# Kernel optimization log

Measured on AMD Instinct MI355X. Metric: run time of the kernel, lower is better.

The kernel has to match this reference:

```python
import jax, jax.numpy as jnp
import numpy as np

B, D, A = 512, 32, 18          # batch, n_latent_dims (= n_heads), n_actions
FED, AED = 128, 64             # factor/action embed dims
VD = FED + AED                 # vdim = 192
KD = VD                        # kdim (key_embed_dim=None -> vdim)
HID = 256                      # per-head MLP hidden size
H = D                          # n_heads = n_latent_dims


def setup_inputs() -> dict:
    key = jax.random.key(0)
    ks = jax.random.split(key, 20)
    s = lambda i, shape: jax.random.normal(ks[i], shape, dtype=jnp.float32) * 0.05
    return {
        "features": jax.random.normal(ks[0], (B, D), dtype=jnp.float32),
        "actions": jax.random.uniform(ks[1], (B, A), dtype=jnp.float32),
        # linear projections (stored as [in, out], i.e. torch weight.T)
        "Wq": s(2, (A, KD)),  "bq": s(3, (KD,)),      # action_query_projection
        "Wk": s(4, (D, KD)),  "bk": s(5, (KD,)),      # factor_key_projection
        "Wav": s(6, (A, AED)), "bav": s(7, (AED,)),   # action_val_projection
        "Wfv": s(8, (D, FED)), "bfv": s(9, (FED,)),   # factor_val_projection
        # per-head input MLPs: vdim -> HID -> vdim (ReLU)
        "W1": s(10, (H, VD, HID)), "b1": s(11, (H, HID)),
        "W2": s(12, (H, HID, VD)), "b2": s(13, (H, VD)),
        # per-head output MLPs: vdim -> HID -> 1 (ReLU)
        "W1o": s(14, (H, VD, HID)), "b1o": s(15, (H, HID)),
        "W2o": s(16, (H, HID)),     "b2o": s(17, (H,)),
    }


def reference(features, actions, Wq, bq, Wk, bk, Wav, bav, Wfv, bfv,
              W1, b1, W2, b2, W1o, b1o, W2o, b2o):
    z, a = features, actions
    # diag_embed(z) row i = z_i * e_i, so Linear(diag_embed(z))[..., i, :] = z_i * W.T[i] + b.
    # z is expanded identically across heads, so factor embeds/keys are head-independent.
    factor_embeds = z[:, :, None] * Wfv[None] + bfv          # [B, D, FED]
    keys = z[:, :, None] * Wk[None] + bk                     # [B, D, KD]
    queries = a @ Wq + bq                                    # [B, KD]
    action_embeds = a @ Wav + bav                            # [B, AED]

    # concat factor vals with broadcast action vals -> [B, D, VD]
    cv = jnp.concatenate(
        [factor_embeds, jnp.broadcast_to(action_embeds[:, None, :], (B, D, AED))], axis=-1)

    # per-head input MLPs (ReLU), batched over heads via einsum
    h = jax.nn.relu(jnp.einsum('bdv,hvk->bhdk', cv, W1) + b1[None, :, None, :])
    values = jnp.einsum('bhdk,hkv->bhdv', h, W2) + b2[None, :, None, :]  # [B,H,D,VD]

    # attention: single query vs D keys; head-independent weights
    scores = (keys @ queries[:, :, None])[..., 0] / jnp.sqrt(jnp.float32(KD))  # [B, D]
    w = jax.nn.softmax(scores, axis=-1)                       # [B, D]
    attn_out = jnp.einsum('bd,bhdv->bhv', w, values)          # [B, H, VD]

    # per-head output MLPs (ReLU) -> scalar effect per head
    h2 = jax.nn.relu(jnp.einsum('bhv,hvk->bhk', attn_out, W1o) + b1o[None])
    effect = jnp.einsum('bhk,hk->bh', h2, W2o) + b2o[None]    # [B, H]

    attn_weights = jnp.broadcast_to(w[:, None, :], (B, H, D))  # [B, H, D]
    return effect, attn_weights
```

## Files before the change

kernel.cpp:

```cpp
#include <hip/hip_runtime.h>
#include <hip/hip_bf16.h>


typedef __attribute__((ext_vector_type(8))) short bf16x8;
typedef __attribute__((ext_vector_type(4))) short bf16x4;
typedef __attribute__((ext_vector_type(4))) float f32x4;

__device__ __forceinline__ short f2bf(float x) {
  unsigned u = __float_as_uint(x);
  u += 0x7fffu + ((u >> 16) & 1u);
  return (short)(u >> 16);
}

__global__ __launch_bounds__(256) void kA_prep(
    const float* __restrict__ feat, const float* __restrict__ act,
    const float* __restrict__ Wq, const float* __restrict__ bq,
    const float* __restrict__ Wk,
    const float* __restrict__ Wav, const float* __restrict__ bav,
    const float* __restrict__ Wfv, const float* __restrict__ bfv,
    const float* __restrict__ W1, const float* __restrict__ b1,
    const float* __restrict__ W2, const float* __restrict__ b2,
    const float* __restrict__ W1o, const float* __restrict__ b1o,
    float* __restrict__ ws_w, float* __restrict__ ws_U,
    float* __restrict__ ws_c0, unsigned short* __restrict__ ws_Mbf,
    float* __restrict__ ws_c1, float* __restrict__ ws_W1g,
    float* __restrict__ out_aw) {
  __shared__ float sh[8448];
  const int bx = blockIdx.x;
  const int t = threadIdx.x;

  if (bx < 64) {
    const int b0 = bx * 8;
    float* sWk = sh;
    float* sA  = sh + 6144;
    float* sQk = sh + 6320;
    float* sW  = sh + 6944;
#pragma unroll
    for (int i = 0; i < 24; ++i) {
      const int idx = i * 256 + t;
      sWk[(idx % 192) * 32 + (idx / 192)] = Wk[idx];
    }
    if (t < 144) sA[t] = act[b0 * 18 + t];
    __syncthreads();
    for (int o = t; o < 608; o += 256) {
      const int j = o >> 5, d = o & 31;
      const float* arow = (j < 18) ? (Wq + j * 192) : bq;
      float acc = 0.f;
      for (int c = 0; c < 192; ++c) acc += arow[c] * sWk[c * 32 + d];
      sQk[o] = acc;
    }
    __syncthreads();
    {
      const int bi = t >> 5, d = t & 31;
      float dot = sQk[18 * 32 + d];
#pragma unroll
      for (int j = 0; j < 18; ++j) dot += sA[bi * 18 + j] * sQk[j * 32 + d];
      const float z = feat[b0 * 32 + t];
      float sc = z * dot * 0.07216878364870322f;
      float mx = sc;
#pragma unroll
      for (int off = 16; off >= 1; off >>= 1) mx = fmaxf(mx, __shfl_xor(mx, off, 64));
      const float e = __expf(sc - mx);
      float s = e;
#pragma unroll
      for (int off = 16; off >= 1; off >>= 1) s += __shfl_xor(s, off, 64);
      const float w = e / s;
      ws_w[b0 * 32 + t] = w;
      sW[t] = w;
    }
    __syncthreads();
#pragma unroll
    for (int i = 0; i < 32; ++i)
      out_aw[b0 * 1024 + i * 256 + t] = sW[(i >> 2) * 32 + (t & 31)];

  } else if (bx < 224) {
    const int r = bx - 64;
    const int h = r / 5, dt = r % 5;
    float* sF = sh;
    if (dt < 4) {
#pragma unroll
      for (int i = 0; i < 4; ++i) sF[i * 256 + t] = Wfv[dt * 1024 + i * 256 + t];
    } else {
      if (t < 128) sF[t] = bfv[t];
    }
    __syncthreads();
    if (dt < 4) {
      float acc[8];
#pragma unroll
      for (int dd = 0; dd < 8; ++dd) acc[dd] = 0.f;
#pragma unroll 4
      for (int fc = 0; fc < 32; ++fc) {
        float w1v[4];
#pragma unroll
        for (int u = 0; u < 4; ++u) w1v[u] = W1[(h * 192 + fc * 4 + u) * 256 + t];
#pragma unroll
        for (int dd = 0; dd < 8; ++dd) {
          float4 f4 = *(const float4*)(sF + dd * 128 + fc * 4);
          acc[dd] += f4.x * w1v[0] + f4.y * w1v[1] + f4.z * w1v[2] + f4.w * w1v[3];
        }
      }
#pragma unroll
      for (int dd = 0; dd < 8; ++dd)
        ws_U[(h * 32 + dt * 8 + dd) * 256 + t] = acc[dd];
    } else {
      float acc = b1[h * 256 + t];
      for (int fc = 0; fc < 32; ++fc) {
        float w1v[4];
#pragma unroll
        for (int u = 0; u < 4; ++u) w1v[u] = W1[(h * 192 + fc * 4 + u) * 256 + t];
        float4 f4 = *(const float4*)(sF + fc * 4);
        acc += f4.x * w1v[0] + f4.y * w1v[1] + f4.z * w1v[2] + f4.w * w1v[3];
      }
      for (int u = 0; u < 64; ++u)
        acc += bav[u] * W1[(h * 192 + 128 + u) * 256 + t];
      ws_c0[h * 256 + t] = acc;
    }

  } else if (bx < 736) {
    const int r = bx - 224;
    const int h = r >> 4, kt = r & 15;
    float* s = sh;
    if (t < 192) {
#pragma unroll
      for (int rr = 0; rr < 16; ++rr)
        s[rr * 200 + t] = W2[h * 49152 + kt * 3072 + rr * 192 + t];
    }
    __syncthreads();
    const int k2q = t >> 2, rq = t & 3;
    float acc[4][4];
#pragma unroll
    for (int r0 = 0; r0 < 4; ++r0)
#pragma unroll
      for (int c = 0; c < 4; ++c) acc[r0][c] = 0.f;
    float c1acc[4] = {0.f, 0.f, 0.f, 0.f};
    const float* W1op = W1o + h * 49152 + k2q * 4;
#pragma unroll 4
    for (int vc = 0; vc < 48; ++vc) {
      float w1q[4][4];
#pragma unroll
      for (int u = 0; u < 4; ++u) {
        float4 w4 = *(const float4*)(W1op + (vc * 4 + u) * 256);
        w1q[u][0] = w4.x; w1q[u][1] = w4.y; w1q[u][2] = w4.z; w1q[u][3] = w4.w;
      }
      float w2q[4][4];
#pragma unroll
      for (int r0 = 0; r0 < 4; ++r0) {
        float4 w2 = *(const float4*)(s + (rq * 4 + r0) * 200 + vc * 4);
        w2q[r0][0] = w2.x; w2q[r0][1] = w2.y; w2q[r0][2] = w2.z; w2q[r0][3] = w2.w;
      }
      float b2v[4];
#pragma unroll
      for (int u = 0; u < 4; ++u) b2v[u] = b2[h * 192 + vc * 4 + u];
#pragma unroll
      for (int u = 0; u < 4; ++u) {
#pragma unroll
        for (int c = 0; c < 4; ++c) c1acc[c] += b2v[u] * w1q[u][c];
#pragma unroll
        for (int r0 = 0; r0 < 4; ++r0)
#pragma unroll
          for (int c = 0; c < 4; ++c)
            acc[r0][c] += w2q[r0][u] * w1q[u][c];
      }
    }
#pragma unroll
    for (int c = 0; c < 4; ++c) {
      bf16x4 p;
#pragma unroll
      for (int r0 = 0; r0 < 4; ++r0) p[r0] = f2bf(acc[r0][c]);
      *(bf16x4*)(ws_Mbf + (size_t)(h * 256 + k2q * 4 + c) * 256 + kt * 16 + rq * 4) = p;
    }
    if (kt == 0 && rq == 0) {
#pragma unroll
      for (int c = 0; c < 4; ++c)
        ws_c1[h * 256 + k2q * 4 + c] = c1acc[c] + b1o[h * 256 + k2q * 4 + c];
    }

  } else {
    const int h = bx - 736;
    float accj[18];
#pragma unroll
    for (int j = 0; j < 18; ++j) accj[j] = 0.f;
#pragma unroll 4
    for (int u = 0; u < 64; ++u) {
      const float w1v = W1[(h * 192 + 128 + u) * 256 + t];
#pragma unroll
      for (int j = 0; j < 18; ++j)
        accj[j] += Wav[j * 64 + u] * w1v;
    }
#pragma unroll
    for (int j = 0; j < 18; ++j)
      ws_W1g[(h * 20 + j) * 256 + t] = accj[j];
    ws_W1g[(h * 20 + 18) * 256 + t] = 0.f;
    ws_W1g[(h * 20 + 19) * 256 + t] = 0.f;
  }
}

__global__ __launch_bounds__(256) void kB_main(
    const float* __restrict__ feat, const float* __restrict__ act,
    const float* __restrict__ ws_w, const float* __restrict__ ws_U,
    const float* __restrict__ ws_W1g, const float* __restrict__ ws_c0,
    const unsigned short* __restrict__ ws_Mbf, const float* __restrict__ ws_c1,
    const float* __restrict__ W2o, const float* __restrict__ b2o,
    float* __restrict__ out_eff) {
  const int bx = blockIdx.x;
  const int h = (bx & 7) * 4 + ((bx >> 3) & 3);
  const int bt = bx >> 5;
  const int b0 = bt * 16;
  const int t = threadIdx.x;

  __shared__ __align__(16) char smem[14208];
  short* sP   = (short*)smem;
  float* sA   = (float*)(smem + 8448);
  float* sZ   = (float*)(smem + 9728);
  float* sWw  = (float*)(smem + 11776);
  float* sRed = (float*)(smem + 13824);

  {
#pragma unroll
    for (int i = 0; i < 2; ++i) {
      sZ[i * 256 + t]  = feat[b0 * 32 + i * 256 + t];
      sWw[i * 256 + t] = ws_w[b0 * 32 + i * 256 + t];
    }
    for (int i = t; i < 320; i += 256) {
      const int row = i / 20, col = i - row * 20;
      sA[i] = (col < 18) ? act[(b0 + row) * 18 + col] : 0.f;
    }
  }
  __syncthreads();

  {
    const int bq = t >> 6, kg = t & 63;
    float g[4][4];

    {
      float4 c04 = *(const float4*)(ws_c0 + h * 256 + kg * 4);
#pragma unroll
      for (int r = 0; r < 4; ++r) {
        g[r][0] = c04.x; g[r][1] = c04.y; g[r][2] = c04.z; g[r][3] = c04.w;
      }
      const float* Wgp = ws_W1g + (h * 20) * 256 + kg * 4;
#pragma unroll
      for (int jc = 0; jc < 5; ++jc) {
        float w1q[4][4];
#pragma unroll
        for (int u = 0; u < 4; ++u) {
          float4 w4 = *(const float4*)(Wgp + (jc * 4 + u) * 256);
          w1q[u][0] = w4.x; w1q[u][1] = w4.y; w1q[u][2] = w4.z; w1q[u][3] = w4.w;
        }
        float a4[4][4];
#pragma unroll
        for (int r = 0; r < 4; ++r) {
          float4 av = *(const float4*)(sA + (bq * 4 + r) * 20 + jc * 4);
          a4[r][0] = av.x; a4[r][1] = av.y; a4[r][2] = av.z; a4[r][3] = av.w;
        }
#pragma unroll
        for (int u = 0; u < 4; ++u)
#pragma unroll
          for (int r = 0; r < 4; ++r)
#pragma unroll
            for (int c = 0; c < 4; ++c)
              g[r][c] += a4[r][u] * w1q[u][c];
      }
    }

    float acc[4][4];
#pragma unroll
    for (int r = 0; r < 4; ++r) {
      acc[r][0] = 0.f; acc[r][1] = 0.f; acc[r][2] = 0.f; acc[r][3] = 0.f;
    }
    const float* Up = ws_U + h * 8192 + kg * 4;
#pragma unroll
    for (int dc = 0; dc < 8; ++dc) {
      float uc[4][4];
#pragma unroll
      for (int dd = 0; dd < 4; ++dd) {
        float4 u4 = *(const float4*)(Up + (dc * 4 + dd) * 256);
        uc[dd][0] = u4.x; uc[dd][1] = u4.y; uc[dd][2] = u4.z; uc[dd][3] = u4.w;
      }
      float zr[4][4], wr[4][4];
#pragma unroll
      for (int r = 0; r < 4; ++r) {
        float4 z4 = *(const float4*)(sZ + (bq * 4 + r) * 32 + dc * 4);
        float4 w4 = *(const float4*)(sWw + (bq * 4 + r) * 32 + dc * 4);
        zr[r][0] = z4.x; zr[r][1] = z4.y; zr[r][2] = z4.z; zr[r][3] = z4.w;
        wr[r][0] = w4.x; wr[r][1] = w4.y; wr[r][2] = w4.z; wr[r][3] = w4.w;
      }
#pragma unroll
      for (int dd = 0; dd < 4; ++dd) {
#pragma unroll
        for (int r = 0; r < 4; ++r) {
#pragma unroll
          for (int c = 0; c < 4; ++c)
            acc[r][c] += wr[r][dd] * fmaxf(zr[r][dd] * uc[dd][c] + g[r][c], 0.f);
        }
      }
    }
#pragma unroll
    for (int r = 0; r < 4; ++r) {
      bf16x4 p;
#pragma unroll
      for (int c = 0; c < 4; ++c) p[c] = f2bf(acc[r][c]);
      *(bf16x4*)(sP + (bq * 4 + r) * 264 + kg * 4) = p;
    }
  }
  __syncthreads();

  {
    const int wv = t >> 6;
    const int lane = t & 63;
    const int quad = lane >> 4, l15 = lane & 15;

    f32x4 acc[4];
    const f32x4 zero = {0.f, 0.f, 0.f, 0.f};
#pragma unroll
    for (int nt = 0; nt < 4; ++nt) acc[nt] = zero;

    float c1r[4], w2r[4];
#pragma unroll
    for (int nt = 0; nt < 4; ++nt) {
      const int col = wv * 64 + nt * 16 + l15;
      c1r[nt] = ws_c1[h * 256 + col];
      w2r[nt] = W2o[h * 256 + col];
    }
    const unsigned short* Mp = ws_Mbf + (size_t)(h * 256 + wv * 64) * 256;

#pragma unroll
    for (int kc = 0; kc < 8; ++kc) {
      bf16x8 a0 = *(const bf16x8*)(sP + l15 * 264 + kc * 32 + quad * 8);
      bf16x8 bfr[4];
#pragma unroll
      for (int nt = 0; nt < 4; ++nt)
        bfr[nt] = *(const bf16x8*)(Mp + (nt * 16 + l15) * 256 + kc * 32 + quad * 8);
#pragma unroll
      for (int nt = 0; nt < 4; ++nt)
        acc[nt] = __builtin_amdgcn_mfma_f32_16x16x32_bf16(a0, bfr[nt], acc[nt], 0, 0, 0);
    }
#pragma unroll
    for (int r = 0; r < 4; ++r) {
      float s = fmaxf(acc[0][r] + c1r[0], 0.f) * w2r[0]
              + fmaxf(acc[1][r] + c1r[1], 0.f) * w2r[1]
              + fmaxf(acc[2][r] + c1r[2], 0.f) * w2r[2]
              + fmaxf(acc[3][r] + c1r[3], 0.f) * w2r[3];
      s += __shfl_xor(s, 1, 64);
      s += __shfl_xor(s, 2, 64);
      s += __shfl_xor(s, 4, 64);
      s += __shfl_xor(s, 8, 64);
      if (l15 == 0) sRed[(quad * 4 + r) * 4 + wv] = s;
    }
  }
  __syncthreads();
  if (t < 16) {
    float v = sRed[t * 4] + sRed[t * 4 + 1] + sRed[t * 4 + 2] + sRed[t * 4 + 3] + b2o[h];
    out_eff[(b0 + t) * 32 + h] = v;
  }
}

extern "C" void kernel_launch(void* const* d_in, const int* in_sizes, int n_in,
                              void* d_out, int out_size, void* d_ws, size_t ws_size,
                              hipStream_t stream) {
  const float* feat = (const float*)d_in[0];
  const float* act  = (const float*)d_in[1];
  const float* Wq   = (const float*)d_in[2];
  const float* bq   = (const float*)d_in[3];
  const float* Wk   = (const float*)d_in[4];
  const float* Wav  = (const float*)d_in[6];
  const float* bav  = (const float*)d_in[7];
  const float* Wfv  = (const float*)d_in[8];
  const float* bfv  = (const float*)d_in[9];
  const float* W1   = (const float*)d_in[10];
  const float* b1   = (const float*)d_in[11];
  const float* W2   = (const float*)d_in[12];
  const float* b2   = (const float*)d_in[13];
  const float* W1o  = (const float*)d_in[14];
  const float* b1o  = (const float*)d_in[15];
  const float* W2o  = (const float*)d_in[16];
  const float* b2o  = (const float*)d_in[17];
  float* out = (float*)d_out;
  float* ws = (float*)d_ws;

  float* ws_w  = ws;
  float* ws_U  = ws + 16384;
  float* ws_c0 = ws + 278528;
  float* ws_c1 = ws + 286720;
  unsigned short* ws_Mbf = (unsigned short*)(ws + 294912);
  float* ws_W1g = ws + 1343488;

  hipLaunchKernelGGL(kA_prep, dim3(768), dim3(256), 0, stream,
                     feat, act, Wq, bq, Wk, Wav, bav, Wfv, bfv, W1, b1,
                     W2, b2, W1o, b1o, ws_w, ws_U, ws_c0, ws_Mbf, ws_c1,
                     ws_W1g, out + 16384);
  hipLaunchKernelGGL(kB_main, dim3(1024), dim3(256), 0, stream,
                     feat, act, ws_w, ws_U, ws_W1g, ws_c0, ws_Mbf, ws_c1,
                     W2o, b2o, out);
}
```

Before: 153.1 us.

## Compute folded W2·W1o weight product with bf16 MFMA instead of scalar FMA

```diff
diff --git a/kernel.cpp b/kernel.cpp
--- a/kernel.cpp
+++ b/kernel.cpp
@@ -10,6 +10,9 @@
   unsigned u = __float_as_uint(x);
   u += 0x7fffu + ((u >> 16) & 1u);
   return (short)(u >> 16);
+}
+__device__ __forceinline__ float bf2f(unsigned short u) {
+  return __uint_as_float((unsigned)u << 16);
 }
 
 __global__ __launch_bounds__(256) void kA_prep(
@@ -25,7 +28,8 @@
     float* __restrict__ ws_c0, unsigned short* __restrict__ ws_Mbf,
     float* __restrict__ ws_c1, float* __restrict__ ws_W1g,
     float* __restrict__ out_aw) {
-  __shared__ float sh[8448];
+  __shared__ __align__(16) char smem[33792];
+  float* sh = (float*)smem;
   const int bx = blockIdx.x;
   const int t = threadIdx.x;
 
@@ -116,67 +120,73 @@
       ws_c0[h * 256 + t] = acc;
     }
 
-  } else if (bx < 736) {
+  } else if (bx < 480) {
     const int r = bx - 224;
-    const int h = r >> 4, kt = r & 15;
-    float* s = sh;
-    if (t < 192) {
-#pragma unroll
-      for (int rr = 0; rr < 16; ++rr)
-        s[rr * 200 + t] = W2[h * 49152 + kt * 3072 + rr * 192 + t];
-    }
-    __syncthreads();
-    const int k2q = t >> 2, rq = t & 3;
-    float acc[4][4];
-#pragma unroll
-    for (int r0 = 0; r0 < 4; ++r0)
-#pragma unroll
-      for (int c = 0; c < 4; ++c) acc[r0][c] = 0.f;
-    float c1acc[4] = {0.f, 0.f, 0.f, 0.f};
-    const float* W1op = W1o + h * 49152 + k2q * 4;
-#pragma unroll 4
-    for (int vc = 0; vc < 48; ++vc) {
-      float w1q[4][4];
-#pragma unroll
-      for (int u = 0; u < 4; ++u) {
-        float4 w4 = *(const float4*)(W1op + (vc * 4 + u) * 256);
-        w1q[u][0] = w4.x; w1q[u][1] = w4.y; w1q[u][2] = w4.z; w1q[u][3] = w4.w;
-      }
-      float w2q[4][4];
-#pragma unroll
-      for (int r0 = 0; r0 < 4; ++r0) {
-        float4 w2 = *(const float4*)(s + (rq * 4 + r0) * 200 + vc * 4);
-        w2q[r0][0] = w2.x; w2q[r0][1] = w2.y; w2q[r0][2] = w2.z; w2q[r0][3] = w2.w;
-      }
-      float b2v[4];
-#pragma unroll
-      for (int u = 0; u < 4; ++u) b2v[u] = b2[h * 192 + vc * 4 + u];
-#pragma unroll
-      for (int u = 0; u < 4; ++u) {
-#pragma unroll
-        for (int c = 0; c < 4; ++c) c1acc[c] += b2v[u] * w1q[u][c];
-#pragma unroll
-        for (int r0 = 0; r0 < 4; ++r0)
-#pragma unroll
-          for (int c = 0; c < 4; ++c)
-            acc[r0][c] += w2q[r0][u] * w1q[u][c];
-      }
-    }
-#pragma unroll
-    for (int c = 0; c < 4; ++c) {
-      bf16x4 p;
-#pragma unroll
-      for (int r0 = 0; r0 < 4; ++r0) p[r0] = f2bf(acc[r0][c]);
-      *(bf16x4*)(ws_Mbf + (size_t)(h * 256 + k2q * 4 + c) * 256 + kt * 16 + rq * 4) = p;
-    }
-    if (kt == 0 && rq == 0) {
-#pragma unroll
-      for (int c = 0; c < 4; ++c)
-        ws_c1[h * 256 + k2q * 4 + c] = c1acc[c] + b1o[h * 256 + k2q * 4 + c];
-    }
+    const int h = r >> 3, kt = r & 7;
+    short* sW2 = (short*)smem;
+    short* sB  = (short*)(smem + 13184);
+
+    for (int i = t; i < 6144; i += 256) {
+      const int row = i / 192, col = i - row * 192;
+      sW2[row * 206 + col] = f2bf(W2[h * 49152 + (kt * 32 + row) * 192 + col]);
+    }
+    const int wv = t >> 6, lane = t & 63;
+    const int quad = lane >> 4, l15 = lane & 15;
+
+    f32x4 acc[2][4];
+    const f32x4 zero = {0.f, 0.f, 0.f, 0.f};
+#pragma unroll
+    for (int mt = 0; mt < 2; ++mt)
+#pragma unroll
+      for (int nt = 0; nt < 4; ++nt) acc[mt][nt] = zero;
+    float c1acc = 0.f;
+
+    for (int kk = 0; kk < 6; ++kk) {
+      __syncthreads();
+#pragma unroll
+      for (int vp = 0; vp < 32; vp += 2) {
+        const float f0 = W1o[h * 49152 + (kk * 32 + vp) * 256 + t];
+        const float f1 = W1o[h * 49152 + (kk * 32 + vp + 1) * 256 + t];
+        const unsigned pack =
+            ((unsigned)(unsigned short)f2bf(f1) << 16) | (unsigned short)f2bf(f0);
+        *(unsigned*)(sB + t * 38 + vp) = pack;
+      }
+      __syncthreads();
+      if (kt == 0) {
+#pragma unroll
+        for (int vp = 0; vp < 32; ++vp)
+          c1acc += b2[h * 192 + kk * 32 + vp] * bf2f((unsigned short)sB[t * 38 + vp]);
+      }
+      bf16x8 a0[2];
+#pragma unroll
+      for (int mt = 0; mt < 2; ++mt)
+        a0[mt] = *(const bf16x8*)(sW2 + (mt * 16 + l15) * 206 + kk * 32 + quad * 8);
+#pragma unroll
+      for (int nt = 0; nt < 4; ++nt) {
+        bf16x8 b0 = *(const bf16x8*)(sB + (wv * 64 + nt * 16 + l15) * 38 + quad * 8);
+#pragma unroll
+        for (int mt = 0; mt < 2; ++mt)
+          acc[mt][nt] = __builtin_amdgcn_mfma_f32_16x16x32_bf16(a0[mt], b0, acc[mt][nt], 0, 0, 0);
+      }
+    }
+#pragma unroll
+    for (int mt = 0; mt < 2; ++mt) {
+#pragma unroll
+      for (int nt = 0; nt < 4; ++nt) {
+        const int col = wv * 64 + nt * 16 + l15;
+        const unsigned p0 = ((unsigned)(unsigned short)f2bf(acc[mt][nt][1]) << 16) |
+                            (unsigned short)f2bf(acc[mt][nt][0]);
+        const unsigned p1 = ((unsigned)(unsigned short)f2bf(acc[mt][nt][3]) << 16) |
+                            (unsigned short)f2bf(acc[mt][nt][2]);
+        unsigned* dst = (unsigned*)(ws_Mbf + (size_t)(h * 256 + col) * 256 +
+                                    kt * 32 + mt * 16 + quad * 4);
+        dst[0] = p0; dst[1] = p1;
+      }
+    }
+    if (kt == 0) ws_c1[h * 256 + t] = c1acc + b1o[h * 256 + t];
 
   } else {
-    const int h = bx - 736;
+    const int h = bx - 480;
     float accj[18];
 #pragma unroll
     for (int j = 0; j < 18; ++j) accj[j] = 0.f;
@@ -385,7 +395,7 @@
   unsigned short* ws_Mbf = (unsigned short*)(ws + 294912);
   float* ws_W1g = ws + 1343488;
 
-  hipLaunchKernelGGL(kA_prep, dim3(768), dim3(256), 0, stream,
+  hipLaunchKernelGGL(kA_prep, dim3(512), dim3(256), 0, stream,
                      feat, act, Wq, bq, Wk, Wav, bav, Wfv, bfv, W1, b1,
                      W2, b2, W1o, b1o, ws_w, ws_U, ws_c0, ws_Mbf, ws_c1,
                      ws_W1g, out + 16384);
```

Result: faster. 146.3 us (-4.4%).
